# Kernel optimization log

Measured on AMD Instinct MI355X. Metric: run time of the kernel, lower is better.

The kernel has to match this reference:

```python
import jax, jax.numpy as jnp
import numpy as np

N = 16384       # input points
D_IN = 64       # feature dim
D_OUT = 128     # output dim
STRIDE = 4      # downsampling stride -> M = N // STRIDE sampled points
NSAMPLE = 16    # hard-coded in __init__
BN_EPS = 1e-5


def setup_inputs() -> dict:
    key = jax.random.key(0)
    k1, k2, k3 = jax.random.split(key, 3)
    p = jax.random.normal(k1, (N, 3), jnp.float32)
    x = jax.random.normal(k2, (N, D_IN), jnp.float32)
    o = jnp.array([N], jnp.int32)  # single-cloud offsets
    # mlp params: Linear(d_in+3, d_out) + BatchNorm1d(d_out)
    W = jax.random.normal(k3, (D_IN + 3, D_OUT), jnp.float32) * 0.05
    b = jnp.zeros((D_OUT,), jnp.float32)
    gamma = jnp.ones((D_OUT,), jnp.float32)
    beta = jnp.zeros((D_OUT,), jnp.float32)
    return {"p": p, "x": x, "o": o, "W": W, "b": b, "gamma": gamma, "beta": beta}


def fps(p, m):
    """Furthest point sampling: returns m indices into p [N,3]. Sequential by nature."""
    n = p.shape[0]
    dists = jnp.full((n,), jnp.inf, p.dtype)
    idxs = jnp.zeros((m,), jnp.int32)  # start from point 0 (pointops convention)

    def body(i, carry):
        idxs, dists = carry
        last = p[idxs[i - 1]]                      # [3]
        d = jnp.sum((p - last) ** 2, axis=1)       # [N]
        dists = jnp.minimum(dists, d)
        return idxs.at[i].set(jnp.argmax(dists).astype(jnp.int32)), dists

    idxs, _ = jax.lax.fori_loop(1, m, body, (idxs, dists))
    return idxs


def reference(p, x, o, W, b, gamma, beta):
    m = p.shape[0] // STRIDE  # static
    # --- furthest point sampling (non-differentiable index op, as in pointops) ---
    s_idx = fps(jax.lax.stop_gradient(p), m)
    n_p = p[s_idx]                                             # [M,3]
    # --- query-and-group: kNN of each sampled point over all N points ---
    d2 = (jnp.sum(n_p ** 2, axis=1)[:, None]
          + jnp.sum(p ** 2, axis=1)[None, :]
          - 2.0 * n_p @ p.T)                                   # [M,N]
    _, nn_idx = jax.lax.top_k(-d2, NSAMPLE)                    # [M,K]
    pj = p[nn_idx] - n_p[:, None, :]                           # [M,K,3] relative coords
    xj = x[nn_idx]                                             # [M,K,D_IN]
    # normalize relative coords by max neighbor norm per sampled point
    nrm = jnp.linalg.norm(pj, axis=-1, keepdims=True)          # [M,K,1]
    pj = pj / (jnp.max(nrm, axis=1, keepdims=True) + 1e-8)
    feat = jnp.concatenate([pj, xj], axis=-1).max(axis=1)      # [M, 3+D_IN] max-pool
    # --- MLP: Linear + BatchNorm1d (training stats) + ReLU ---
    h = feat @ W + b                                           # [M, D_OUT]
    mean = jnp.mean(h, axis=0)
    var = jnp.var(h, axis=0)
    h = (h - mean) / jnp.sqrt(var + BN_EPS) * gamma + beta
    x_out = jax.nn.relu(h)
    n_o = jnp.array([m], jnp.int32)
    return (n_p, x_out, n_o)
```

## Files before the change

### kernel.cpp

```cpp
#include <hip/hip_runtime.h>

#define N_PTS 16384
#define M_PTS 4096
#define D_INF 64
#define D_OUTF 128
#define KNN 16
#define DF 67

__global__ __launch_bounds__(256) void sp_kernel(const float* __restrict__ p,
                                                 float* __restrict__ spn) {
  int j = blockIdx.x * 256 + threadIdx.x;
  float a = p[3 * j], b = p[3 * j + 1], c = p[3 * j + 2];
  spn[j] = __fadd_rn(__fadd_rn(__fmul_rn(a, a), __fmul_rn(b, b)), __fmul_rn(c, c));
}

#define FPS_T 512
#define FPS_PPT 32

__global__ __launch_bounds__(FPS_T, 2) void fps_kernel(const float* __restrict__ p,
                                                       int* __restrict__ sidx,
                                                       float* __restrict__ np_out) {
  const int t = threadIdx.x;
  float px[FPS_PPT], py[FPS_PPT], pz[FPS_PPT], dd[FPS_PPT];
#pragma unroll
  for (int k = 0; k < FPS_PPT; ++k) {
    int j = t + (k << 9);
    px[k] = p[3 * j]; py[k] = p[3 * j + 1]; pz[k] = p[3 * j + 2];
    dd[k] = INFINITY;
  }
  __shared__ float s_v[2][FPS_T / 64];
  __shared__ int   s_i[2][FPS_T / 64];
  if (t == 0) {
    sidx[0] = 0;
    np_out[0] = p[0]; np_out[1] = p[1]; np_out[2] = p[2];
  }
  float lx = p[0], ly = p[1], lz = p[2];
  for (int i = 1; i < M_PTS; ++i) {
    float tmax = -INFINITY;
#pragma unroll
    for (int k = 0; k < FPS_PPT; ++k) {
      float dx = __fsub_rn(px[k], lx);
      float dy = __fsub_rn(py[k], ly);
      float dz = __fsub_rn(pz[k], lz);
      float d = __fadd_rn(__fadd_rn(__fmul_rn(dx, dx), __fmul_rn(dy, dy)),
                          __fmul_rn(dz, dz));
      float nd = fminf(dd[k], d);
      dd[k] = nd;
      tmax = fmaxf(tmax, nd);
    }
    int bk = 0;
#pragma unroll
    for (int k = FPS_PPT - 1; k >= 0; --k) {
      if (dd[k] == tmax) bk = k;
    }
    int ri = t + (bk << 9);
    float rv = tmax;
#pragma unroll
    for (int off = 32; off >= 1; off >>= 1) {
      float ov = __shfl_xor(rv, off);
      int   oi = __shfl_xor(ri, off);
      bool tk = (ov > rv) || (ov == rv && oi < ri);
      rv = tk ? ov : rv;
      ri = tk ? oi : ri;
    }
    const int par = i & 1;
    if ((t & 63) == 0) { s_v[par][t >> 6] = rv; s_i[par][t >> 6] = ri; }
    __syncthreads();
    float gv = s_v[par][0];
    int   gi = s_i[par][0];
#pragma unroll
    for (int w = 1; w < FPS_T / 64; ++w) {
      float ov = s_v[par][w];
      int   oi = s_i[par][w];
      bool tk = (ov > gv) || (ov == gv && oi < gi);
      gv = tk ? ov : gv;
      gi = tk ? oi : gi;
    }
    lx = p[3 * gi]; ly = p[3 * gi + 1]; lz = p[3 * gi + 2];
    if (t == 0) {
      sidx[i] = gi;
      np_out[3 * i] = lx; np_out[3 * i + 1] = ly; np_out[3 * i + 2] = lz;
    }
  }
}

__global__ __launch_bounds__(256) void knn_feat_kernel(const float* __restrict__ p,
                                                       const float* __restrict__ x,
                                                       const float* __restrict__ spn,
                                                       const int* __restrict__ sidx,
                                                       float* __restrict__ feat) {
  __shared__ float cd[4][256];
  __shared__ int ci[4][256];
  __shared__ int cnt[4];
  __shared__ int s_nn[4][KNN];
  const int w = threadIdx.x >> 6;
  const int lane = threadIdx.x & 63;
  const int q = (blockIdx.x << 2) + w;
  const int qi = sidx[q];
  const float qx = p[3 * qi], qy = p[3 * qi + 1], qz = p[3 * qi + 2];
  const float sn = spn[qi];
  if (lane == 0) cnt[w] = 0;
  float lmin = INFINITY;
  for (int it = 0; it < N_PTS / 64; ++it) {
    int j = lane + (it << 6);
    float dot = __fmaf_rn(qz, p[3 * j + 2],
                 __fmaf_rn(qy, p[3 * j + 1], __fmul_rn(qx, p[3 * j])));
    float d2 = __fsub_rn(__fadd_rn(sn, spn[j]), __fmul_rn(2.0f, dot));
    lmin = fminf(lmin, d2);
  }
  float mv = lmin;
  float tau = INFINITY;
#pragma unroll
  for (int r = 0; r < KNN; ++r) {
    float rmin = mv;
#pragma unroll
    for (int off = 32; off >= 1; off >>= 1) rmin = fminf(rmin, __shfl_xor(rmin, off));
    tau = rmin;
    unsigned long long msk = __ballot(mv == rmin);
    if (lane == (int)(__ffsll(msk) - 1)) mv = INFINITY;
  }
  __syncthreads();
  for (int it = 0; it < N_PTS / 64; ++it) {
    int j = lane + (it << 6);
    float dot = __fmaf_rn(qz, p[3 * j + 2],
                 __fmaf_rn(qy, p[3 * j + 1], __fmul_rn(qx, p[3 * j])));
    float d2 = __fsub_rn(__fadd_rn(sn, spn[j]), __fmul_rn(2.0f, dot));
    if (d2 <= tau) {
      int pos = atomicAdd(&cnt[w], 1);
      if (pos < 256) { cd[w][pos] = d2; ci[w][pos] = j; }
    }
  }
  __syncthreads();
  int C = min(cnt[w], 256);
  float vv[4]; int ii[4];
#pragma unroll
  for (int s = 0; s < 4; ++s) {
    int pos = lane + (s << 6);
    bool ok = pos < C;
    vv[s] = ok ? cd[w][pos] : INFINITY;
    ii[s] = ok ? ci[w][pos] : 0x7FFFFFFF;
  }
#pragma unroll
  for (int r = 0; r < KNN; ++r) {
    float bv = vv[0]; int bi = ii[0]; int bs = 0;
#pragma unroll
    for (int s = 1; s < 4; ++s) {
      bool tk = (vv[s] < bv) || (vv[s] == bv && ii[s] < bi);
      bv = tk ? vv[s] : bv; bi = tk ? ii[s] : bi; bs = tk ? s : bs;
    }
    float rv = bv; int ri = bi;
#pragma unroll
    for (int off = 32; off >= 1; off >>= 1) {
      float ov = __shfl_xor(rv, off); int oi = __shfl_xor(ri, off);
      bool tk = (ov < rv) || (ov == rv && oi < ri);
      rv = tk ? ov : rv; ri = tk ? oi : ri;
    }
    if (bi == ri) {
#pragma unroll
      for (int s = 0; s < 4; ++s) if (s == bs) vv[s] = INFINITY;
    }
    if (lane == 0) s_nn[w][r] = ri;
  }
  __syncthreads();
  float ax = -INFINITY, ay = -INFINITY, az = -INFINITY, nr = -INFINITY;
  if (lane < KNN) {
    int jn = s_nn[w][lane];
    ax = __fsub_rn(p[3 * jn], qx);
    ay = __fsub_rn(p[3 * jn + 1], qy);
    az = __fsub_rn(p[3 * jn + 2], qz);
    nr = sqrtf(__fadd_rn(__fadd_rn(__fmul_rn(ax, ax), __fmul_rn(ay, ay)),
                         __fmul_rn(az, az)));
  }
  float mnr = nr, mx = ax, my = ay, mz = az;
#pragma unroll
  for (int off = 32; off >= 1; off >>= 1) {
    mnr = fmaxf(mnr, __shfl_xor(mnr, off));
    mx = fmaxf(mx, __shfl_xor(mx, off));
    my = fmaxf(my, __shfl_xor(my, off));
    mz = fmaxf(mz, __shfl_xor(mz, off));
  }
  if (lane == 0) {
    float sden = __fadd_rn(mnr, 1e-8f);
    feat[q * DF + 0] = mx / sden;
    feat[q * DF + 1] = my / sden;
    feat[q * DF + 2] = mz / sden;
  }
  float fm = -INFINITY;
#pragma unroll
  for (int k = 0; k < KNN; ++k) {
    int jn = s_nn[w][k];
    fm = fmaxf(fm, x[(jn << 6) + lane]);
  }
  feat[q * DF + 3 + lane] = fm;
}

__global__ __launch_bounds__(128) void mlp_kernel(const float* __restrict__ feat,
                                                  const float* __restrict__ W,
                                                  const float* __restrict__ b,
                                                  float* __restrict__ h) {
  int mrow = blockIdx.x;
  int o = threadIdx.x;
  const float* fr = feat + mrow * DF;
  float acc = b[o];
#pragma unroll
  for (int k = 0; k < DF; ++k) acc = __fmaf_rn(fr[k], W[k * D_OUTF + o], acc);
  h[mrow * D_OUTF + o] = acc;
}

__global__ __launch_bounds__(256) void stats_kernel(const float* __restrict__ h,
                                                    const float* __restrict__ gamma,
                                                    const float* __restrict__ beta,
                                                    float* __restrict__ scsh) {
  int o = blockIdx.x;
  int t = threadIdx.x;
  float s = 0.f, s2 = 0.f;
  for (int mrow = t; mrow < M_PTS; mrow += 256) {
    float v = h[mrow * D_OUTF + o];
    s += v;
    s2 = __fmaf_rn(v, v, s2);
  }
#pragma unroll
  for (int off = 32; off >= 1; off >>= 1) {
    s += __shfl_xor(s, off);
    s2 += __shfl_xor(s2, off);
  }
  __shared__ float as1[4], as2[4];
  if ((t & 63) == 0) { as1[t >> 6] = s; as2[t >> 6] = s2; }
  __syncthreads();
  if (t == 0) {
    float ts = ((as1[0] + as1[1]) + as1[2]) + as1[3];
    float ts2 = ((as2[0] + as2[1]) + as2[2]) + as2[3];
    float mean = ts / (float)M_PTS;
    float var = ts2 / (float)M_PTS - mean * mean;
    var = fmaxf(var, 0.f);
    float sc = gamma[o] / sqrtf(var + 1e-5f);
    scsh[o] = sc;
    scsh[D_OUTF + o] = beta[o] - mean * sc;
  }
}

__global__ __launch_bounds__(256) void bn_kernel(const float* __restrict__ h,
                                                 const float* __restrict__ scsh,
                                                 float* __restrict__ out) {
  int idx = blockIdx.x * 256 + threadIdx.x;
  int o = idx & (D_OUTF - 1);
  float v = __fmaf_rn(h[idx], scsh[o], scsh[D_OUTF + o]);
  out[M_PTS * 3 + idx] = fmaxf(v, 0.f);
  if (idx == 0) out[M_PTS * 3 + M_PTS * D_OUTF] = 4096.0f;
}

extern "C" void kernel_launch(void* const* d_in, const int* in_sizes, int n_in,
                              void* d_out, int out_size, void* d_ws, size_t ws_size,
                              hipStream_t stream) {
  const float* p     = (const float*)d_in[0];
  const float* x     = (const float*)d_in[1];
  const float* W     = (const float*)d_in[3];
  const float* b     = (const float*)d_in[4];
  const float* gamma = (const float*)d_in[5];
  const float* beta  = (const float*)d_in[6];
  float* out = (float*)d_out;

  float* wsf  = (float*)d_ws;
  int*   sidx = (int*)d_ws;
  float* spn  = wsf + 4096;
  float* feat = spn + N_PTS;
  float* h    = feat + M_PTS * DF;
  float* scsh = h + M_PTS * D_OUTF;

  sp_kernel<<<N_PTS / 256, 256, 0, stream>>>(p, spn);
  fps_kernel<<<1, FPS_T, 0, stream>>>(p, sidx, out);
  knn_feat_kernel<<<M_PTS / 4, 256, 0, stream>>>(p, x, spn, sidx, feat);
  mlp_kernel<<<M_PTS, D_OUTF, 0, stream>>>(feat, W, b, h);
  stats_kernel<<<D_OUTF, 256, 0, stream>>>(h, gamma, beta, scsh);
  bn_kernel<<<(M_PTS * D_OUTF) / 256, 256, 0, stream>>>(h, scsh, out);
}
```

Before: 8.623 ms.

## Widen FPS block to 1024 threads and pass winner coords via shuffle/LDS

```diff
diff --git a/kernel.cpp b/kernel.cpp
--- a/kernel.cpp
+++ b/kernel.cpp
@@ -14,22 +14,26 @@
   spn[j] = __fadd_rn(__fadd_rn(__fmul_rn(a, a), __fmul_rn(b, b)), __fmul_rn(c, c));
 }
 
-#define FPS_T 512
-#define FPS_PPT 32
-
-__global__ __launch_bounds__(FPS_T, 2) void fps_kernel(const float* __restrict__ p,
+#define FPS_T 1024
+#define FPS_PPT 16
+#define FPS_W (FPS_T / 64)
+
+typedef float vf16 __attribute__((ext_vector_type(16)));
+
+__global__ __launch_bounds__(FPS_T, 4) void fps_kernel(const float* __restrict__ p,
                                                        int* __restrict__ sidx,
                                                        float* __restrict__ np_out) {
   const int t = threadIdx.x;
-  float px[FPS_PPT], py[FPS_PPT], pz[FPS_PPT], dd[FPS_PPT];
+  vf16 px, py, pz, dd;
 #pragma unroll
   for (int k = 0; k < FPS_PPT; ++k) {
-    int j = t + (k << 9);
+    int j = t + (k << 10);
     px[k] = p[3 * j]; py[k] = p[3 * j + 1]; pz[k] = p[3 * j + 2];
     dd[k] = INFINITY;
   }
-  __shared__ float s_v[2][FPS_T / 64];
-  __shared__ int   s_i[2][FPS_T / 64];
+  __shared__ float s_v[2][FPS_W];
+  __shared__ int   s_i[2][FPS_W];
+  __shared__ float s_x[2][FPS_W], s_y[2][FPS_W], s_z[2][FPS_W];
   if (t == 0) {
     sidx[0] = 0;
     np_out[0] = p[0]; np_out[1] = p[1]; np_out[2] = p[2];
@@ -48,12 +52,12 @@
       dd[k] = nd;
       tmax = fmaxf(tmax, nd);
     }
-    int bk = 0;
+    int ri = 0x7FFFFFFF;
+    float cx = 0.f, cy = 0.f, cz = 0.f;
 #pragma unroll
     for (int k = FPS_PPT - 1; k >= 0; --k) {
-      if (dd[k] == tmax) bk = k;
-    }
-    int ri = t + (bk << 9);
+      if (dd[k] == tmax) { ri = t + (k << 10); cx = px[k]; cy = py[k]; cz = pz[k]; }
+    }
     float rv = tmax;
 #pragma unroll
     for (int off = 32; off >= 1; off >>= 1) {
@@ -63,20 +67,30 @@
       rv = tk ? ov : rv;
       ri = tk ? oi : ri;
     }
+    int src = ri & 63;
+    float wx = __shfl(cx, src);
+    float wy = __shfl(cy, src);
+    float wz = __shfl(cz, src);
     const int par = i & 1;
-    if ((t & 63) == 0) { s_v[par][t >> 6] = rv; s_i[par][t >> 6] = ri; }
+    if ((t & 63) == 0) {
+      int w = t >> 6;
+      s_v[par][w] = rv; s_i[par][w] = ri;
+      s_x[par][w] = wx; s_y[par][w] = wy; s_z[par][w] = wz;
+    }
     __syncthreads();
     float gv = s_v[par][0];
     int   gi = s_i[par][0];
-#pragma unroll
-    for (int w = 1; w < FPS_T / 64; ++w) {
+    int   gw = 0;
+#pragma unroll
+    for (int w = 1; w < FPS_W; ++w) {
       float ov = s_v[par][w];
       int   oi = s_i[par][w];
       bool tk = (ov > gv) || (ov == gv && oi < gi);
       gv = tk ? ov : gv;
       gi = tk ? oi : gi;
-    }
-    lx = p[3 * gi]; ly = p[3 * gi + 1]; lz = p[3 * gi + 2];
+      gw = tk ? w : gw;
+    }
+    lx = s_x[par][gw]; ly = s_y[par][gw]; lz = s_z[par][gw];
     if (t == 0) {
       sidx[i] = gi;
       np_out[3 * i] = lx; np_out[3 * i + 1] = ly; np_out[3 * i + 2] = lz;
```

After: 13.45 ms. 56.0% more time.

## Split furthest point sampling across eight blocks with global flag synchronization

Applied to the files above, without the earlier changes.

```diff
diff --git a/kernel.cpp b/kernel.cpp
--- a/kernel.cpp
+++ b/kernel.cpp
@@ -8,76 +8,120 @@
 #define DF 67
 
 __global__ __launch_bounds__(256) void sp_kernel(const float* __restrict__ p,
-                                                 float* __restrict__ spn) {
+                                                 float* __restrict__ spn,
+                                                 float4* __restrict__ sp4,
+                                                 unsigned int* __restrict__ tags) {
   int j = blockIdx.x * 256 + threadIdx.x;
   float a = p[3 * j], b = p[3 * j + 1], c = p[3 * j + 2];
   spn[j] = __fadd_rn(__fadd_rn(__fmul_rn(a, a), __fmul_rn(b, b)), __fmul_rn(c, c));
-}
-
-#define FPS_T 512
-#define FPS_PPT 32
-
-__global__ __launch_bounds__(FPS_T, 2) void fps_kernel(const float* __restrict__ p,
-                                                       int* __restrict__ sidx,
-                                                       float* __restrict__ np_out) {
+  sp4[j] = make_float4(a, b, c, 0.f);
+  if (j < 128) tags[j] = 0;
+}
+
+#define FPS_NB 8
+#define FPS_BT 512
+
+__global__ __launch_bounds__(FPS_BT) void fps_kernel(
+    const float4* __restrict__ sp4, const float* __restrict__ p,
+    int* __restrict__ sidx, float* __restrict__ np_out,
+    unsigned int* __restrict__ tags, float* __restrict__ slots) {
   const int t = threadIdx.x;
-  float px[FPS_PPT], py[FPS_PPT], pz[FPS_PPT], dd[FPS_PPT];
-#pragma unroll
-  for (int k = 0; k < FPS_PPT; ++k) {
-    int j = t + (k << 9);
-    px[k] = p[3 * j]; py[k] = p[3 * j + 1]; pz[k] = p[3 * j + 2];
-    dd[k] = INFINITY;
-  }
-  __shared__ float s_v[2][FPS_T / 64];
-  __shared__ int   s_i[2][FPS_T / 64];
-  if (t == 0) {
+  const int b = blockIdx.x;
+  const int lane = t & 63;
+  const int w = t >> 6;
+  const int base = b << 11;
+  float4 q0 = sp4[base + t];
+  float4 q1 = sp4[base + 512 + t];
+  float4 q2 = sp4[base + 1024 + t];
+  float4 q3 = sp4[base + 1536 + t];
+  float dd0 = INFINITY, dd1 = INFINITY, dd2 = INFINITY, dd3 = INFINITY;
+  __shared__ float s_loc[8][8];
+  __shared__ float s_glob[8][8];
+  float lx = p[0], ly = p[1], lz = p[2];
+  if (b == 0 && t == 0) {
     sidx[0] = 0;
-    np_out[0] = p[0]; np_out[1] = p[1]; np_out[2] = p[2];
-  }
-  float lx = p[0], ly = p[1], lz = p[2];
+    np_out[0] = lx; np_out[1] = ly; np_out[2] = lz;
+  }
   for (int i = 1; i < M_PTS; ++i) {
-    float tmax = -INFINITY;
-#pragma unroll
-    for (int k = 0; k < FPS_PPT; ++k) {
-      float dx = __fsub_rn(px[k], lx);
-      float dy = __fsub_rn(py[k], ly);
-      float dz = __fsub_rn(pz[k], lz);
-      float d = __fadd_rn(__fadd_rn(__fmul_rn(dx, dx), __fmul_rn(dy, dy)),
-                          __fmul_rn(dz, dz));
-      float nd = fminf(dd[k], d);
-      dd[k] = nd;
-      tmax = fmaxf(tmax, nd);
-    }
-    int bk = 0;
-#pragma unroll
-    for (int k = FPS_PPT - 1; k >= 0; --k) {
-      if (dd[k] == tmax) bk = k;
-    }
-    int ri = t + (bk << 9);
-    float rv = tmax;
+    float tv = -INFINITY; int ti = 0x7FFFFFFF;
+    float tx = 0.f, ty = 0.f, tz = 0.f;
+#define FPS_STEPQ(Q, DD, K)                                                   \
+  do {                                                                        \
+    float dx = __fsub_rn(Q.x, lx);                                            \
+    float dy = __fsub_rn(Q.y, ly);                                            \
+    float dz = __fsub_rn(Q.z, lz);                                            \
+    float d = __fadd_rn(__fadd_rn(__fmul_rn(dx, dx), __fmul_rn(dy, dy)),      \
+                        __fmul_rn(dz, dz));                                   \
+    float nd = fminf(DD, d);                                                  \
+    DD = nd;                                                                  \
+    bool gt = nd > tv;                                                        \
+    tv = gt ? nd : tv;                                                        \
+    ti = gt ? (base + ((K) << 9) + t) : ti;                                   \
+    tx = gt ? Q.x : tx; ty = gt ? Q.y : ty; tz = gt ? Q.z : tz;               \
+  } while (0)
+    FPS_STEPQ(q0, dd0, 0);
+    FPS_STEPQ(q1, dd1, 1);
+    FPS_STEPQ(q2, dd2, 2);
+    FPS_STEPQ(q3, dd3, 3);
+    float rv = tv; int ri = ti; float rx = tx, ry = ty, rz = tz;
 #pragma unroll
     for (int off = 32; off >= 1; off >>= 1) {
       float ov = __shfl_xor(rv, off);
       int   oi = __shfl_xor(ri, off);
+      float ox = __shfl_xor(rx, off);
+      float oy = __shfl_xor(ry, off);
+      float oz = __shfl_xor(rz, off);
       bool tk = (ov > rv) || (ov == rv && oi < ri);
-      rv = tk ? ov : rv;
-      ri = tk ? oi : ri;
-    }
-    const int par = i & 1;
-    if ((t & 63) == 0) { s_v[par][t >> 6] = rv; s_i[par][t >> 6] = ri; }
+      rv = tk ? ov : rv; ri = tk ? oi : ri;
+      rx = tk ? ox : rx; ry = tk ? oy : ry; rz = tk ? oz : rz;
+    }
+    if (lane == 0) {
+      s_loc[w][0] = rv; s_loc[w][1] = __int_as_float(ri);
+      s_loc[w][2] = rx; s_loc[w][3] = ry; s_loc[w][4] = rz;
+    }
     __syncthreads();
-    float gv = s_v[par][0];
-    int   gi = s_i[par][0];
-#pragma unroll
-    for (int w = 1; w < FPS_T / 64; ++w) {
-      float ov = s_v[par][w];
-      int   oi = s_i[par][w];
+    if (t == 0) {
+      float bv = s_loc[0][0]; int bi = __float_as_int(s_loc[0][1]);
+      float bx = s_loc[0][2], by = s_loc[0][3], bz = s_loc[0][4];
+#pragma unroll
+      for (int w2 = 1; w2 < 8; ++w2) {
+        float ov = s_loc[w2][0]; int oi = __float_as_int(s_loc[w2][1]);
+        bool tk = (ov > bv) || (ov == bv && oi < bi);
+        bv = tk ? ov : bv; bi = tk ? oi : bi;
+        bx = tk ? s_loc[w2][2] : bx;
+        by = tk ? s_loc[w2][3] : by;
+        bz = tk ? s_loc[w2][4] : bz;
+      }
+      float* sl = slots + (((i & 1) * FPS_NB + b) << 4);
+      sl[0] = bv; sl[1] = __int_as_float(bi);
+      sl[2] = bx; sl[3] = by; sl[4] = bz;
+      __threadfence();
+      __hip_atomic_store(&tags[b << 4], (unsigned int)i,
+                         __ATOMIC_RELEASE, __HIP_MEMORY_SCOPE_AGENT);
+    }
+    if (t < FPS_NB) {
+      unsigned int v = __hip_atomic_load(&tags[t << 4], __ATOMIC_ACQUIRE,
+                                         __HIP_MEMORY_SCOPE_AGENT);
+      int guard = 0;
+      while (v < (unsigned int)i) {
+        if (++guard > (1 << 26)) break;
+        v = __hip_atomic_load(&tags[t << 4], __ATOMIC_ACQUIRE,
+                              __HIP_MEMORY_SCOPE_AGENT);
+      }
+      const float* sl = slots + (((i & 1) * FPS_NB + t) << 4);
+      s_glob[t][0] = sl[0]; s_glob[t][1] = sl[1];
+      s_glob[t][2] = sl[2]; s_glob[t][3] = sl[3]; s_glob[t][4] = sl[4];
+    }
+    __syncthreads();
+    float gv = s_glob[0][0]; int gi = __float_as_int(s_glob[0][1]); int gw = 0;
+#pragma unroll
+    for (int b2 = 1; b2 < 8; ++b2) {
+      float ov = s_glob[b2][0]; int oi = __float_as_int(s_glob[b2][1]);
       bool tk = (ov > gv) || (ov == gv && oi < gi);
-      gv = tk ? ov : gv;
-      gi = tk ? oi : gi;
-    }
-    lx = p[3 * gi]; ly = p[3 * gi + 1]; lz = p[3 * gi + 2];
-    if (t == 0) {
+      gv = tk ? ov : gv; gi = tk ? oi : gi; gw = tk ? b2 : gw;
+    }
+    lx = s_glob[gw][2]; ly = s_glob[gw][3]; lz = s_glob[gw][4];
+    if (b == 0 && t == 0) {
       sidx[i] = gi;
       np_out[3 * i] = lx; np_out[3 * i + 1] = ly; np_out[3 * i + 2] = lz;
     }
@@ -267,8 +311,12 @@
   float* h    = feat + M_PTS * DF;
   float* scsh = h + M_PTS * D_OUTF;
 
-  sp_kernel<<<N_PTS / 256, 256, 0, stream>>>(p, spn);
-  fps_kernel<<<1, FPS_T, 0, stream>>>(p, sidx, out);
+  float4* sp4        = (float4*)h;
+  unsigned int* tags = (unsigned int*)feat;
+  float* slots       = feat + 128;
+
+  sp_kernel<<<N_PTS / 256, 256, 0, stream>>>(p, spn, sp4, tags);
+  fps_kernel<<<FPS_NB, FPS_BT, 0, stream>>>(sp4, p, sidx, out, tags, slots);
   knn_feat_kernel<<<M_PTS / 4, 256, 0, stream>>>(p, x, spn, sidx, feat);
   mlp_kernel<<<M_PTS, D_OUTF, 0, stream>>>(feat, W, b, h);
   stats_kernel<<<D_OUTF, 256, 0, stream>>>(h, gamma, beta, scsh);
```

Result: slower. 14.40 ms (+67.0%).

## Move FPS xy coordinates to LDS and carry winner z through reduction

Applied to the files above, without the earlier changes.

```diff
diff --git a/kernel.cpp b/kernel.cpp
--- a/kernel.cpp
+++ b/kernel.cpp
@@ -15,46 +15,86 @@
 }
 
 #define FPS_T 512
-#define FPS_PPT 32
-
-__global__ __launch_bounds__(FPS_T, 2) void fps_kernel(const float* __restrict__ p,
-                                                       int* __restrict__ sidx,
-                                                       float* __restrict__ np_out) {
+#define FPS_W (FPS_T / 64)
+
+__global__ __launch_bounds__(FPS_T) void fps_kernel(const float* __restrict__ p,
+                                                    int* __restrict__ sidx,
+                                                    float* __restrict__ np_out) {
   const int t = threadIdx.x;
-  float px[FPS_PPT], py[FPS_PPT], pz[FPS_PPT], dd[FPS_PPT];
-#pragma unroll
-  for (int k = 0; k < FPS_PPT; ++k) {
-    int j = t + (k << 9);
-    px[k] = p[3 * j]; py[k] = p[3 * j + 1]; pz[k] = p[3 * j + 2];
-    dd[k] = INFINITY;
-  }
-  __shared__ float s_v[2][FPS_T / 64];
-  __shared__ int   s_i[2][FPS_T / 64];
+  __shared__ float2 s_xy[N_PTS];
+  __shared__ float4 s_red[2][FPS_W];
+  float4 z0, z1, z2, z3, z4, z5, z6, z7;
+  float4 d0, d1, d2, d3, d4, d5, d6, d7;
+
+#define FPS_LD(ZF, DF_, K)                                           \
+  do {                                                               \
+    int j = t + ((K) << 9);                                          \
+    s_xy[j] = make_float2(p[3 * j], p[3 * j + 1]);                   \
+    ZF = p[3 * j + 2];                                               \
+    DF_ = INFINITY;                                                  \
+  } while (0)
+
+  FPS_LD(z0.x, d0.x, 0);  FPS_LD(z0.y, d0.y, 1);  FPS_LD(z0.z, d0.z, 2);  FPS_LD(z0.w, d0.w, 3);
+  FPS_LD(z1.x, d1.x, 4);  FPS_LD(z1.y, d1.y, 5);  FPS_LD(z1.z, d1.z, 6);  FPS_LD(z1.w, d1.w, 7);
+  FPS_LD(z2.x, d2.x, 8);  FPS_LD(z2.y, d2.y, 9);  FPS_LD(z2.z, d2.z, 10); FPS_LD(z2.w, d2.w, 11);
+  FPS_LD(z3.x, d3.x, 12); FPS_LD(z3.y, d3.y, 13); FPS_LD(z3.z, d3.z, 14); FPS_LD(z3.w, d3.w, 15);
+  FPS_LD(z4.x, d4.x, 16); FPS_LD(z4.y, d4.y, 17); FPS_LD(z4.z, d4.z, 18); FPS_LD(z4.w, d4.w, 19);
+  FPS_LD(z5.x, d5.x, 20); FPS_LD(z5.y, d5.y, 21); FPS_LD(z5.z, d5.z, 22); FPS_LD(z5.w, d5.w, 23);
+  FPS_LD(z6.x, d6.x, 24); FPS_LD(z6.y, d6.y, 25); FPS_LD(z6.z, d6.z, 26); FPS_LD(z6.w, d6.w, 27);
+  FPS_LD(z7.x, d7.x, 28); FPS_LD(z7.y, d7.y, 29); FPS_LD(z7.z, d7.z, 30); FPS_LD(z7.w, d7.w, 31);
+
   if (t == 0) {
     sidx[0] = 0;
     np_out[0] = p[0]; np_out[1] = p[1]; np_out[2] = p[2];
   }
   float lx = p[0], ly = p[1], lz = p[2];
+  __syncthreads();
+
   for (int i = 1; i < M_PTS; ++i) {
     float tmax = -INFINITY;
-#pragma unroll
-    for (int k = 0; k < FPS_PPT; ++k) {
-      float dx = __fsub_rn(px[k], lx);
-      float dy = __fsub_rn(py[k], ly);
-      float dz = __fsub_rn(pz[k], lz);
-      float d = __fadd_rn(__fadd_rn(__fmul_rn(dx, dx), __fmul_rn(dy, dy)),
-                          __fmul_rn(dz, dz));
-      float nd = fminf(dd[k], d);
-      dd[k] = nd;
-      tmax = fmaxf(tmax, nd);
-    }
-    int bk = 0;
-#pragma unroll
-    for (int k = FPS_PPT - 1; k >= 0; --k) {
-      if (dd[k] == tmax) bk = k;
-    }
-    int ri = t + (bk << 9);
+#define FPS_UPD(ZF, DF_, K)                                                   \
+  do {                                                                        \
+    float2 xy = s_xy[t + ((K) << 9)];                                         \
+    float dx = __fsub_rn(xy.x, lx);                                           \
+    float dy = __fsub_rn(xy.y, ly);                                           \
+    float dz = __fsub_rn(ZF, lz);                                             \
+    float d = __fadd_rn(__fadd_rn(__fmul_rn(dx, dx), __fmul_rn(dy, dy)),      \
+                        __fmul_rn(dz, dz));                                   \
+    float nd = fminf(DF_, d);                                                 \
+    DF_ = nd;                                                                 \
+    tmax = fmaxf(tmax, nd);                                                   \
+  } while (0)
+
+    FPS_UPD(z0.x, d0.x, 0);  FPS_UPD(z0.y, d0.y, 1);  FPS_UPD(z0.z, d0.z, 2);  FPS_UPD(z0.w, d0.w, 3);
+    FPS_UPD(z1.x, d1.x, 4);  FPS_UPD(z1.y, d1.y, 5);  FPS_UPD(z1.z, d1.z, 6);  FPS_UPD(z1.w, d1.w, 7);
+    FPS_UPD(z2.x, d2.x, 8);  FPS_UPD(z2.y, d2.y, 9);  FPS_UPD(z2.z, d2.z, 10); FPS_UPD(z2.w, d2.w, 11);
+    FPS_UPD(z3.x, d3.x, 12); FPS_UPD(z3.y, d3.y, 13); FPS_UPD(z3.z, d3.z, 14); FPS_UPD(z3.w, d3.w, 15);
+    FPS_UPD(z4.x, d4.x, 16); FPS_UPD(z4.y, d4.y, 17); FPS_UPD(z4.z, d4.z, 18); FPS_UPD(z4.w, d4.w, 19);
+    FPS_UPD(z5.x, d5.x, 20); FPS_UPD(z5.y, d5.y, 21); FPS_UPD(z5.z, d5.z, 22); FPS_UPD(z5.w, d5.w, 23);
+    FPS_UPD(z6.x, d6.x, 24); FPS_UPD(z6.y, d6.y, 25); FPS_UPD(z6.z, d6.z, 26); FPS_UPD(z6.w, d6.w, 27);
+    FPS_UPD(z7.x, d7.x, 28); FPS_UPD(z7.y, d7.y, 29); FPS_UPD(z7.z, d7.z, 30); FPS_UPD(z7.w, d7.w, 31);
+
+    int kk = 0;
+    float bz = 0.f;
+#define FPS_RSC(ZF, DF_, K)                        \
+  do {                                             \
+    bool c = (DF_ == tmax);                        \
+    kk = c ? (K) : kk;                             \
+    bz = c ? ZF : bz;                              \
+  } while (0)
+
+    FPS_RSC(z7.w, d7.w, 31); FPS_RSC(z7.z, d7.z, 30); FPS_RSC(z7.y, d7.y, 29); FPS_RSC(z7.x, d7.x, 28);
+    FPS_RSC(z6.w, d6.w, 27); FPS_RSC(z6.z, d6.z, 26); FPS_RSC(z6.y, d6.y, 25); FPS_RSC(z6.x, d6.x, 24);
+    FPS_RSC(z5.w, d5.w, 23); FPS_RSC(z5.z, d5.z, 22); FPS_RSC(z5.y, d5.y, 21); FPS_RSC(z5.x, d5.x, 20);
+    FPS_RSC(z4.w, d4.w, 19); FPS_RSC(z4.z, d4.z, 18); FPS_RSC(z4.y, d4.y, 17); FPS_RSC(z4.x, d4.x, 16);
+    FPS_RSC(z3.w, d3.w, 15); FPS_RSC(z3.z, d3.z, 14); FPS_RSC(z3.y, d3.y, 13); FPS_RSC(z3.x, d3.x, 12);
+    FPS_RSC(z2.w, d2.w, 11); FPS_RSC(z2.z, d2.z, 10); FPS_RSC(z2.y, d2.y, 9);  FPS_RSC(z2.x, d2.x, 8);
+    FPS_RSC(z1.w, d1.w, 7);  FPS_RSC(z1.z, d1.z, 6);  FPS_RSC(z1.y, d1.y, 5);  FPS_RSC(z1.x, d1.x, 4);
+    FPS_RSC(z0.w, d0.w, 3);  FPS_RSC(z0.z, d0.z, 2);  FPS_RSC(z0.y, d0.y, 1);  FPS_RSC(z0.x, d0.x, 0);
+
+    const int my_ri = t + (kk << 9);
     float rv = tmax;
+    int   ri = my_ri;
 #pragma unroll
     for (int off = 32; off >= 1; off >>= 1) {
       float ov = __shfl_xor(rv, off);
@@ -64,19 +104,23 @@
       ri = tk ? oi : ri;
     }
     const int par = i & 1;
-    if ((t & 63) == 0) { s_v[par][t >> 6] = rv; s_i[par][t >> 6] = ri; }
+    if (tmax == rv && my_ri == ri) {
+      s_red[par][t >> 6] = make_float4(rv, __int_as_float(ri), bz, 0.f);
+    }
     __syncthreads();
-    float gv = s_v[par][0];
-    int   gi = s_i[par][0];
-#pragma unroll
-    for (int w = 1; w < FPS_T / 64; ++w) {
-      float ov = s_v[par][w];
-      int   oi = s_i[par][w];
+    float4 e0 = s_red[par][0];
+    float gv = e0.x; int gi = __float_as_int(e0.y); float gz = e0.z;
+#pragma unroll
+    for (int w2 = 1; w2 < FPS_W; ++w2) {
+      float4 e = s_red[par][w2];
+      float ov = e.x; int oi = __float_as_int(e.y);
       bool tk = (ov > gv) || (ov == gv && oi < gi);
       gv = tk ? ov : gv;
       gi = tk ? oi : gi;
-    }
-    lx = p[3 * gi]; ly = p[3 * gi + 1]; lz = p[3 * gi + 2];
+      gz = tk ? e.z : gz;
+    }
+    float2 wxy = s_xy[gi];
+    lx = wxy.x; ly = wxy.y; lz = gz;
     if (t == 0) {
       sidx[i] = gi;
       np_out[3 * i] = lx; np_out[3 * i + 1] = ly; np_out[3 * i + 2] = lz;
```

Result: slower. 9.510 ms (+10.3%).
